# Kernel tuning notes

Hardware: AMD Instinct MI355X
Metric: run time of the kernel (lower is better)

Reference implementation:

```python
import jax, jax.numpy as jnp
import numpy as np

K = 0.15
MOMENTUM = 0.99998
B, C, H, W = 8, 19, 512, 1024


def setup_inputs() -> dict:
    key = jax.random.key(0)
    k1, k2 = jax.random.split(key)
    pred = jax.random.normal(k1, (B, C, H, W), dtype=jnp.float32)
    target = jax.random.randint(k2, (B, H, W), 0, C, dtype=jnp.int32)
    return {"pred": pred, "target": target, "step": 1000}


def reference(pred, target, step):
    b, c, h, w = pred.shape
    # num is a static Python int (step is a Python scalar), matching torch's int(...)
    num = int(K * b * h * w * max(MOMENTUM ** step, K))
    # per-pixel cross entropy, reduction='none': loss[b,h,w] = -log_softmax(pred)[b, target, h, w]
    logp = jax.nn.log_softmax(pred, axis=1)  # [B,C,H,W]
    loss = -jnp.take_along_axis(logp, target[:, None, :, :], axis=1)[:, 0]  # [B,H,W]
    loss = loss.reshape(-1)  # [B*H*W]
    # k-th largest loss value (torch does a full argsort; top_k suffices)
    topv = jax.lax.top_k(loss, num)[0]
    TK = topv[num - 1]
    mask = loss >= TK  # includes ties, like torch's boolean indexing
    return jnp.sum(jnp.where(mask, loss, 0.0)) / jnp.sum(mask).astype(loss.dtype)
```

## Files before the change

kernel.cpp:

```cpp
#include <hip/hip_runtime.h>

#define BB 8
#define CCH 19
#define HH 512
#define WW 1024
#define HW (HH * WW)
#define NPIX (BB * HW)
#define CHW (CCH * HW)
#define N4 (NPIX / 4)

struct SelState {
    unsigned num;
    unsigned b1, k1;
    unsigned b2, k2;
    unsigned tk_key;
};

__device__ __forceinline__ unsigned fkey(float x) {
    unsigned u = __float_as_uint(x);
    return (u & 0x80000000u) ? ~u : (u | 0x80000000u);
}

__global__ void k_num(const int* __restrict__ step_p, SelState* st) {
    if (threadIdx.x == 0 && blockIdx.x == 0) {
        int step = step_p[0];
        double m = pow(0.99998, (double)step);
        double Kc = 0.15;
        double f = m > Kc ? m : Kc;
        double v = Kc * (double)BB * (double)HH * (double)WW * f;
        st->num = (unsigned)v;
    }
}

__global__ __launch_bounds__(256) void k_loss(const float* __restrict__ pred,
                                              const int* __restrict__ target,
                                              float* __restrict__ loss) {
    int i4 = blockIdx.x * 256 + threadIdx.x;
    int p0 = i4 << 2;
    int b = p0 >> 19;
    int hw = p0 & (HW - 1);
    const float* base = pred + (size_t)b * CHW + hw;

    float4 v[CCH];
#pragma unroll
    for (int c = 0; c < CCH; ++c)
        v[c] = *reinterpret_cast<const float4*>(base + (size_t)c * HW);
    int4 tg = *reinterpret_cast<const int4*>(target + p0);

    float4 mx = v[0];
#pragma unroll
    for (int c = 1; c < CCH; ++c) {
        mx.x = fmaxf(mx.x, v[c].x);
        mx.y = fmaxf(mx.y, v[c].y);
        mx.z = fmaxf(mx.z, v[c].z);
        mx.w = fmaxf(mx.w, v[c].w);
    }
    float4 s = make_float4(0.f, 0.f, 0.f, 0.f);
    float4 xt = make_float4(0.f, 0.f, 0.f, 0.f);
#pragma unroll
    for (int c = 0; c < CCH; ++c) {
        s.x += __expf(v[c].x - mx.x);
        s.y += __expf(v[c].y - mx.y);
        s.z += __expf(v[c].z - mx.z);
        s.w += __expf(v[c].w - mx.w);
        xt.x = (tg.x == c) ? v[c].x : xt.x;
        xt.y = (tg.y == c) ? v[c].y : xt.y;
        xt.z = (tg.z == c) ? v[c].z : xt.z;
        xt.w = (tg.w == c) ? v[c].w : xt.w;
    }
    float4 o;
    o.x = __logf(s.x) + mx.x - xt.x;
    o.y = __logf(s.y) + mx.y - xt.y;
    o.z = __logf(s.z) + mx.z - xt.z;
    o.w = __logf(s.w) + mx.w - xt.w;
    *reinterpret_cast<float4*>(loss + p0) = o;
}

__global__ __launch_bounds__(256) void k_histA(const float* __restrict__ loss,
                                               unsigned* __restrict__ hist) {
    __shared__ unsigned h[2048];
    for (int i = threadIdx.x; i < 2048; i += 256) h[i] = 0;
    __syncthreads();
    int stride = gridDim.x * 256;
    for (int i4 = blockIdx.x * 256 + threadIdx.x; i4 < N4; i4 += stride) {
        float4 v = reinterpret_cast<const float4*>(loss)[i4];
        atomicAdd(&h[fkey(v.x) >> 21], 1u);
        atomicAdd(&h[fkey(v.y) >> 21], 1u);
        atomicAdd(&h[fkey(v.z) >> 21], 1u);
        atomicAdd(&h[fkey(v.w) >> 21], 1u);
    }
    __syncthreads();
    for (int i = threadIdx.x; i < 2048; i += 256) {
        unsigned c = h[i];
        if (c) atomicAdd(&hist[i], c);
    }
}

__global__ __launch_bounds__(256) void k_histB(const float* __restrict__ loss,
                                               const SelState* __restrict__ st,
                                               unsigned* __restrict__ hist) {
    __shared__ unsigned h[2048];
    for (int i = threadIdx.x; i < 2048; i += 256) h[i] = 0;
    __syncthreads();
    unsigned b1 = st->b1;
    int stride = gridDim.x * 256;
    for (int i4 = blockIdx.x * 256 + threadIdx.x; i4 < N4; i4 += stride) {
        float4 v = reinterpret_cast<const float4*>(loss)[i4];
        unsigned u;
        u = fkey(v.x); if ((u >> 21) == b1) atomicAdd(&h[(u >> 10) & 2047u], 1u);
        u = fkey(v.y); if ((u >> 21) == b1) atomicAdd(&h[(u >> 10) & 2047u], 1u);
        u = fkey(v.z); if ((u >> 21) == b1) atomicAdd(&h[(u >> 10) & 2047u], 1u);
        u = fkey(v.w); if ((u >> 21) == b1) atomicAdd(&h[(u >> 10) & 2047u], 1u);
    }
    __syncthreads();
    for (int i = threadIdx.x; i < 2048; i += 256) {
        unsigned c = h[i];
        if (c) atomicAdd(&hist[i], c);
    }
}

__global__ __launch_bounds__(256) void k_histC(const float* __restrict__ loss,
                                               const SelState* __restrict__ st,
                                               unsigned* __restrict__ hist) {
    __shared__ unsigned h[1024];
    for (int i = threadIdx.x; i < 1024; i += 256) h[i] = 0;
    __syncthreads();
    unsigned pref22 = (st->b1 << 11) | st->b2;
    int stride = gridDim.x * 256;
    for (int i4 = blockIdx.x * 256 + threadIdx.x; i4 < N4; i4 += stride) {
        float4 v = reinterpret_cast<const float4*>(loss)[i4];
        unsigned u;
        u = fkey(v.x); if ((u >> 10) == pref22) atomicAdd(&h[u & 1023u], 1u);
        u = fkey(v.y); if ((u >> 10) == pref22) atomicAdd(&h[u & 1023u], 1u);
        u = fkey(v.z); if ((u >> 10) == pref22) atomicAdd(&h[u & 1023u], 1u);
        u = fkey(v.w); if ((u >> 10) == pref22) atomicAdd(&h[u & 1023u], 1u);
    }
    __syncthreads();
    for (int i = threadIdx.x; i < 1024; i += 256) {
        unsigned c = h[i];
        if (c) atomicAdd(&hist[i], c);
    }
}

template <int NBINS, int PASS>
__global__ __launch_bounds__(256) void k_scan(const unsigned* __restrict__ hist,
                                              SelState* st) {
    constexpr int PER = NBINS / 256;
    __shared__ unsigned chunk[256];
    int t = threadIdx.x;
    unsigned k = (PASS == 0) ? st->num : (PASS == 1 ? st->k1 : st->k2);

    unsigned local[PER];
    unsigned lsum = 0;
#pragma unroll
    for (int j = 0; j < PER; ++j) { local[j] = hist[t * PER + j]; lsum += local[j]; }
    chunk[t] = lsum;
    __syncthreads();
    for (int off = 1; off < 256; off <<= 1) {
        unsigned add = (t + off < 256) ? chunk[t + off] : 0u;
        __syncthreads();
        chunk[t] += add;
        __syncthreads();
    }
    unsigned cum = (t < 255) ? chunk[t + 1] : 0u;
#pragma unroll
    for (int j = PER - 1; j >= 0; --j) {
        unsigned c = local[j];
        if (k > cum && k <= cum + c) {
            unsigned bin = (unsigned)(t * PER + j);
            unsigned krem = k - cum;
            if (PASS == 0) { st->b1 = bin; st->k1 = krem; }
            else if (PASS == 1) { st->b2 = bin; st->k2 = krem; }
            else { st->tk_key = (st->b1 << 21) | (st->b2 << 10) | bin; }
        }
        cum += c;
    }
}

__global__ __launch_bounds__(256) void k_final(const float* __restrict__ loss,
                                               const SelState* __restrict__ st,
                                               double* __restrict__ psum,
                                               unsigned* __restrict__ pcnt) {
    unsigned tk = st->tk_key;
    double sum = 0.0;
    unsigned cnt = 0;
    int stride = gridDim.x * 256;
    for (int i4 = blockIdx.x * 256 + threadIdx.x; i4 < N4; i4 += stride) {
        float4 v = reinterpret_cast<const float4*>(loss)[i4];
        if (fkey(v.x) >= tk) { sum += (double)v.x; cnt++; }
        if (fkey(v.y) >= tk) { sum += (double)v.y; cnt++; }
        if (fkey(v.z) >= tk) { sum += (double)v.z; cnt++; }
        if (fkey(v.w) >= tk) { sum += (double)v.w; cnt++; }
    }
#pragma unroll
    for (int off = 32; off >= 1; off >>= 1) {
        sum += __shfl_down(sum, off);
        cnt += __shfl_down(cnt, off);
    }
    __shared__ double wsum[4];
    __shared__ unsigned wcnt[4];
    int wid = threadIdx.x >> 6, lane = threadIdx.x & 63;
    if (lane == 0) { wsum[wid] = sum; wcnt[wid] = cnt; }
    __syncthreads();
    if (threadIdx.x == 0) {
        psum[blockIdx.x] = wsum[0] + wsum[1] + wsum[2] + wsum[3];
        pcnt[blockIdx.x] = wcnt[0] + wcnt[1] + wcnt[2] + wcnt[3];
    }
}

__global__ __launch_bounds__(256) void k_finalize(const double* __restrict__ psum,
                                                  const unsigned* __restrict__ pcnt,
                                                  float* __restrict__ out, int nblocks) {
    double s = 0.0;
    unsigned long long c = 0;
    for (int i = threadIdx.x; i < nblocks; i += 256) { s += psum[i]; c += pcnt[i]; }
#pragma unroll
    for (int off = 32; off >= 1; off >>= 1) {
        s += __shfl_down(s, off);
        c += __shfl_down(c, off);
    }
    __shared__ double wsum[4];
    __shared__ unsigned long long wcnt[4];
    int wid = threadIdx.x >> 6, lane = threadIdx.x & 63;
    if (lane == 0) { wsum[wid] = s; wcnt[wid] = c; }
    __syncthreads();
    if (threadIdx.x == 0) {
        double ts = wsum[0] + wsum[1] + wsum[2] + wsum[3];
        unsigned long long tc = wcnt[0] + wcnt[1] + wcnt[2] + wcnt[3];
        out[0] = (float)(ts / (double)tc);
    }
}

extern "C" void kernel_launch(void* const* d_in, const int* in_sizes, int n_in,
                              void* d_out, int out_size, void* d_ws, size_t ws_size,
                              hipStream_t stream) {
    const float* pred = (const float*)d_in[0];
    const int* target = (const int*)d_in[1];
    const int* step = (const int*)d_in[2];
    float* out = (float*)d_out;

    char* ws = (char*)d_ws;
    const size_t LOSS_BYTES = (size_t)NPIX * 4;
    float* loss = (float*)ws;
    unsigned* hist1 = (unsigned*)(ws + LOSS_BYTES);
    unsigned* hist2 = hist1 + 2048;
    unsigned* hist3 = hist2 + 2048;
    SelState* st = (SelState*)(hist3 + 1024);
    double* psum = (double*)(ws + LOSS_BYTES + 20480 + 32);
    unsigned* pcnt = (unsigned*)(psum + 1024);

    hipMemsetAsync(hist1, 0, 20480, stream);

    k_num<<<1, 1, 0, stream>>>(step, st);
    k_loss<<<N4 / 256, 256, 0, stream>>>(pred, target, loss);
    k_histA<<<1024, 256, 0, stream>>>(loss, hist1);
    k_scan<2048, 0><<<1, 256, 0, stream>>>(hist1, st);
    k_histB<<<1024, 256, 0, stream>>>(loss, st, hist2);
    k_scan<2048, 1><<<1, 256, 0, stream>>>(hist2, st);
    k_histC<<<1024, 256, 0, stream>>>(loss, st, hist3);
    k_scan<1024, 2><<<1, 256, 0, stream>>>(hist3, st);
    k_final<<<1024, 256, 0, stream>>>(loss, st, psum, pcnt);
    k_finalize<<<1, 256, 0, stream>>>(psum, pcnt, out, 1024);
}
```

Measured before the change: 138.2 us.

## Fuse loss with first histogram and fold final masked sum into third pass

Computes per-pixel cross-entropy and the first radix histogram in one grid-stride kernel, which removes a full read of the loss buffer. The third histogram pass now also accumulates fixed-point sums and counts for values above the prefix and per-bin sums within it. That lets a single-block kernel finish selection and compute the mean without another pass over the loss. The memset and the separate final and finalize kernels are replaced by a small init kernel. In exchange it adds 64-bit shared and global atomics and fixed-point summation, which assumes non-negative losses and has limited precision.

```diff
diff --git a/kernel.cpp b/kernel.cpp
--- a/kernel.cpp
+++ b/kernel.cpp
@@ -9,11 +9,12 @@
 #define CHW (CCH * HW)
 #define N4 (NPIX / 4)
 
+#define FIX_SCALE 17179869184.0
+
 struct SelState {
     unsigned num;
     unsigned b1, k1;
     unsigned b2, k2;
-    unsigned tk_key;
 };
 
 __device__ __forceinline__ unsigned fkey(float x) {
@@ -21,73 +22,76 @@
     return (u & 0x80000000u) ? ~u : (u | 0x80000000u);
 }
 
-__global__ void k_num(const int* __restrict__ step_p, SelState* st) {
-    if (threadIdx.x == 0 && blockIdx.x == 0) {
+__device__ __forceinline__ unsigned long long fix64(float x) {
+    return (unsigned long long)((double)x * FIX_SCALE);
+}
+
+__global__ __launch_bounds__(256) void k_init(const int* __restrict__ step_p,
+                                              unsigned* __restrict__ zbase,
+                                              SelState* st) {
+    for (int i = threadIdx.x; i < 7172; i += 256) zbase[i] = 0u;
+    if (threadIdx.x == 0) {
         int step = step_p[0];
         double m = pow(0.99998, (double)step);
         double Kc = 0.15;
         double f = m > Kc ? m : Kc;
-        double v = Kc * (double)BB * (double)HH * (double)WW * f;
-        st->num = (unsigned)v;
-    }
-}
-
-__global__ __launch_bounds__(256) void k_loss(const float* __restrict__ pred,
-                                              const int* __restrict__ target,
-                                              float* __restrict__ loss) {
-    int i4 = blockIdx.x * 256 + threadIdx.x;
-    int p0 = i4 << 2;
-    int b = p0 >> 19;
-    int hw = p0 & (HW - 1);
-    const float* base = pred + (size_t)b * CHW + hw;
-
-    float4 v[CCH];
-#pragma unroll
-    for (int c = 0; c < CCH; ++c)
-        v[c] = *reinterpret_cast<const float4*>(base + (size_t)c * HW);
-    int4 tg = *reinterpret_cast<const int4*>(target + p0);
-
-    float4 mx = v[0];
-#pragma unroll
-    for (int c = 1; c < CCH; ++c) {
-        mx.x = fmaxf(mx.x, v[c].x);
-        mx.y = fmaxf(mx.y, v[c].y);
-        mx.z = fmaxf(mx.z, v[c].z);
-        mx.w = fmaxf(mx.w, v[c].w);
-    }
-    float4 s = make_float4(0.f, 0.f, 0.f, 0.f);
-    float4 xt = make_float4(0.f, 0.f, 0.f, 0.f);
-#pragma unroll
-    for (int c = 0; c < CCH; ++c) {
-        s.x += __expf(v[c].x - mx.x);
-        s.y += __expf(v[c].y - mx.y);
-        s.z += __expf(v[c].z - mx.z);
-        s.w += __expf(v[c].w - mx.w);
-        xt.x = (tg.x == c) ? v[c].x : xt.x;
-        xt.y = (tg.y == c) ? v[c].y : xt.y;
-        xt.z = (tg.z == c) ? v[c].z : xt.z;
-        xt.w = (tg.w == c) ? v[c].w : xt.w;
-    }
-    float4 o;
-    o.x = __logf(s.x) + mx.x - xt.x;
-    o.y = __logf(s.y) + mx.y - xt.y;
-    o.z = __logf(s.z) + mx.z - xt.z;
-    o.w = __logf(s.w) + mx.w - xt.w;
-    *reinterpret_cast<float4*>(loss + p0) = o;
-}
-
-__global__ __launch_bounds__(256) void k_histA(const float* __restrict__ loss,
-                                               unsigned* __restrict__ hist) {
+        st->num = (unsigned)(Kc * (double)BB * (double)HH * (double)WW * f);
+    }
+}
+
+__global__ __launch_bounds__(256) void k_loss_hist(const float* __restrict__ pred,
+                                                   const int* __restrict__ target,
+                                                   float* __restrict__ loss,
+                                                   unsigned* __restrict__ hist) {
     __shared__ unsigned h[2048];
     for (int i = threadIdx.x; i < 2048; i += 256) h[i] = 0;
     __syncthreads();
+
     int stride = gridDim.x * 256;
     for (int i4 = blockIdx.x * 256 + threadIdx.x; i4 < N4; i4 += stride) {
-        float4 v = reinterpret_cast<const float4*>(loss)[i4];
-        atomicAdd(&h[fkey(v.x) >> 21], 1u);
-        atomicAdd(&h[fkey(v.y) >> 21], 1u);
-        atomicAdd(&h[fkey(v.z) >> 21], 1u);
-        atomicAdd(&h[fkey(v.w) >> 21], 1u);
+        int p0 = i4 << 2;
+        int b = p0 >> 19;
+        int hw = p0 & (HW - 1);
+        const float* base = pred + (size_t)b * CHW + hw;
+
+        float4 v[CCH];
+#pragma unroll
+        for (int c = 0; c < CCH; ++c)
+            v[c] = *reinterpret_cast<const float4*>(base + (size_t)c * HW);
+        int4 tg = *reinterpret_cast<const int4*>(target + p0);
+
+        float4 mx = v[0];
+#pragma unroll
+        for (int c = 1; c < CCH; ++c) {
+            mx.x = fmaxf(mx.x, v[c].x);
+            mx.y = fmaxf(mx.y, v[c].y);
+            mx.z = fmaxf(mx.z, v[c].z);
+            mx.w = fmaxf(mx.w, v[c].w);
+        }
+        float4 s = make_float4(0.f, 0.f, 0.f, 0.f);
+        float4 xt = make_float4(0.f, 0.f, 0.f, 0.f);
+#pragma unroll
+        for (int c = 0; c < CCH; ++c) {
+            s.x += __expf(v[c].x - mx.x);
+            s.y += __expf(v[c].y - mx.y);
+            s.z += __expf(v[c].z - mx.z);
+            s.w += __expf(v[c].w - mx.w);
+            xt.x = (tg.x == c) ? v[c].x : xt.x;
+            xt.y = (tg.y == c) ? v[c].y : xt.y;
+            xt.z = (tg.z == c) ? v[c].z : xt.z;
+            xt.w = (tg.w == c) ? v[c].w : xt.w;
+        }
+        float4 o;
+        o.x = __logf(s.x) + mx.x - xt.x;
+        o.y = __logf(s.y) + mx.y - xt.y;
+        o.z = __logf(s.z) + mx.z - xt.z;
+        o.w = __logf(s.w) + mx.w - xt.w;
+        *reinterpret_cast<float4*>(loss + p0) = o;
+
+        atomicAdd(&h[fkey(o.x) >> 21], 1u);
+        atomicAdd(&h[fkey(o.y) >> 21], 1u);
+        atomicAdd(&h[fkey(o.z) >> 21], 1u);
+        atomicAdd(&h[fkey(o.w) >> 21], 1u);
     }
     __syncthreads();
     for (int i = threadIdx.x; i < 2048; i += 256) {
@@ -121,39 +125,68 @@
 
 __global__ __launch_bounds__(256) void k_histC(const float* __restrict__ loss,
                                                const SelState* __restrict__ st,
-                                               unsigned* __restrict__ hist) {
+                                               unsigned* __restrict__ h3g,
+                                               unsigned long long* __restrict__ bsg,
+                                               unsigned long long* __restrict__ aboveSum,
+                                               unsigned* __restrict__ aboveCnt) {
     __shared__ unsigned h[1024];
-    for (int i = threadIdx.x; i < 1024; i += 256) h[i] = 0;
+    __shared__ unsigned long long bs[1024];
+    for (int i = threadIdx.x; i < 1024; i += 256) { h[i] = 0; bs[i] = 0ull; }
     __syncthreads();
     unsigned pref22 = (st->b1 << 11) | st->b2;
+    unsigned long long asum = 0ull;
+    unsigned acnt = 0;
     int stride = gridDim.x * 256;
     for (int i4 = blockIdx.x * 256 + threadIdx.x; i4 < N4; i4 += stride) {
         float4 v = reinterpret_cast<const float4*>(loss)[i4];
-        unsigned u;
-        u = fkey(v.x); if ((u >> 10) == pref22) atomicAdd(&h[u & 1023u], 1u);
-        u = fkey(v.y); if ((u >> 10) == pref22) atomicAdd(&h[u & 1023u], 1u);
-        u = fkey(v.z); if ((u >> 10) == pref22) atomicAdd(&h[u & 1023u], 1u);
-        u = fkey(v.w); if ((u >> 10) == pref22) atomicAdd(&h[u & 1023u], 1u);
+        unsigned u, p;
+        u = fkey(v.x); p = u >> 10;
+        if (p > pref22) { asum += fix64(v.x); acnt++; }
+        else if (p == pref22) { atomicAdd(&h[u & 1023u], 1u); atomicAdd(&bs[u & 1023u], fix64(v.x)); }
+        u = fkey(v.y); p = u >> 10;
+        if (p > pref22) { asum += fix64(v.y); acnt++; }
+        else if (p == pref22) { atomicAdd(&h[u & 1023u], 1u); atomicAdd(&bs[u & 1023u], fix64(v.y)); }
+        u = fkey(v.z); p = u >> 10;
+        if (p > pref22) { asum += fix64(v.z); acnt++; }
+        else if (p == pref22) { atomicAdd(&h[u & 1023u], 1u); atomicAdd(&bs[u & 1023u], fix64(v.z)); }
+        u = fkey(v.w); p = u >> 10;
+        if (p > pref22) { asum += fix64(v.w); acnt++; }
+        else if (p == pref22) { atomicAdd(&h[u & 1023u], 1u); atomicAdd(&bs[u & 1023u], fix64(v.w)); }
+    }
+#pragma unroll
+    for (int off = 32; off >= 1; off >>= 1) {
+        asum += __shfl_down(asum, off);
+        acnt += __shfl_down(acnt, off);
+    }
+    __shared__ unsigned long long wsum[4];
+    __shared__ unsigned wcnt[4];
+    int wid = threadIdx.x >> 6, lane = threadIdx.x & 63;
+    if (lane == 0) { wsum[wid] = asum; wcnt[wid] = acnt; }
+    __syncthreads();
+    if (threadIdx.x == 0) {
+        unsigned long long ts = wsum[0] + wsum[1] + wsum[2] + wsum[3];
+        unsigned tc = wcnt[0] + wcnt[1] + wcnt[2] + wcnt[3];
+        if (ts) atomicAdd(aboveSum, ts);
+        if (tc) atomicAdd(aboveCnt, tc);
     }
     __syncthreads();
     for (int i = threadIdx.x; i < 1024; i += 256) {
         unsigned c = h[i];
-        if (c) atomicAdd(&hist[i], c);
-    }
-}
-
-template <int NBINS, int PASS>
+        if (c) { atomicAdd(&h3g[i], c); atomicAdd(&bsg[i], bs[i]); }
+    }
+}
+
+template <int PASS>
 __global__ __launch_bounds__(256) void k_scan(const unsigned* __restrict__ hist,
                                               SelState* st) {
-    constexpr int PER = NBINS / 256;
     __shared__ unsigned chunk[256];
     int t = threadIdx.x;
-    unsigned k = (PASS == 0) ? st->num : (PASS == 1 ? st->k1 : st->k2);
-
-    unsigned local[PER];
+    unsigned k = (PASS == 0) ? st->num : st->k1;
+
+    unsigned local[8];
     unsigned lsum = 0;
 #pragma unroll
-    for (int j = 0; j < PER; ++j) { local[j] = hist[t * PER + j]; lsum += local[j]; }
+    for (int j = 0; j < 8; ++j) { local[j] = hist[t * 8 + j]; lsum += local[j]; }
     chunk[t] = lsum;
     __syncthreads();
     for (int off = 1; off < 256; off <<= 1) {
@@ -164,70 +197,73 @@
     }
     unsigned cum = (t < 255) ? chunk[t + 1] : 0u;
 #pragma unroll
-    for (int j = PER - 1; j >= 0; --j) {
+    for (int j = 7; j >= 0; --j) {
         unsigned c = local[j];
         if (k > cum && k <= cum + c) {
-            unsigned bin = (unsigned)(t * PER + j);
+            unsigned bin = (unsigned)(t * 8 + j);
             unsigned krem = k - cum;
             if (PASS == 0) { st->b1 = bin; st->k1 = krem; }
-            else if (PASS == 1) { st->b2 = bin; st->k2 = krem; }
-            else { st->tk_key = (st->b1 << 21) | (st->b2 << 10) | bin; }
+            else { st->b2 = bin; st->k2 = krem; }
         }
         cum += c;
     }
 }
 
-__global__ __launch_bounds__(256) void k_final(const float* __restrict__ loss,
-                                               const SelState* __restrict__ st,
-                                               double* __restrict__ psum,
-                                               unsigned* __restrict__ pcnt) {
-    unsigned tk = st->tk_key;
-    double sum = 0.0;
+__global__ __launch_bounds__(256) void k_last(const unsigned* __restrict__ h3,
+                                              const unsigned long long* __restrict__ bsg,
+                                              const unsigned long long* __restrict__ aboveSum,
+                                              const unsigned* __restrict__ aboveCnt,
+                                              const SelState* __restrict__ st,
+                                              float* __restrict__ out) {
+    __shared__ unsigned chunk[256];
+    __shared__ unsigned b3sh;
+    __shared__ unsigned long long wsum[4];
+    __shared__ unsigned wcnt[4];
+    int t = threadIdx.x;
+    unsigned k = st->k2;
+
+    unsigned local[4];
+    unsigned lsum = 0;
+#pragma unroll
+    for (int j = 0; j < 4; ++j) { local[j] = h3[t * 4 + j]; lsum += local[j]; }
+    chunk[t] = lsum;
+    __syncthreads();
+    for (int off = 1; off < 256; off <<= 1) {
+        unsigned add = (t + off < 256) ? chunk[t + off] : 0u;
+        __syncthreads();
+        chunk[t] += add;
+        __syncthreads();
+    }
+    unsigned cum = (t < 255) ? chunk[t + 1] : 0u;
+#pragma unroll
+    for (int j = 3; j >= 0; --j) {
+        unsigned c = local[j];
+        if (k > cum && k <= cum + c) b3sh = (unsigned)(t * 4 + j);
+        cum += c;
+    }
+    __syncthreads();
+    unsigned b3 = b3sh;
+
+    unsigned long long s = 0ull;
     unsigned cnt = 0;
-    int stride = gridDim.x * 256;
-    for (int i4 = blockIdx.x * 256 + threadIdx.x; i4 < N4; i4 += stride) {
-        float4 v = reinterpret_cast<const float4*>(loss)[i4];
-        if (fkey(v.x) >= tk) { sum += (double)v.x; cnt++; }
-        if (fkey(v.y) >= tk) { sum += (double)v.y; cnt++; }
-        if (fkey(v.z) >= tk) { sum += (double)v.z; cnt++; }
-        if (fkey(v.w) >= tk) { sum += (double)v.w; cnt++; }
-    }
-#pragma unroll
-    for (int off = 32; off >= 1; off >>= 1) {
-        sum += __shfl_down(sum, off);
-        cnt += __shfl_down(cnt, off);
-    }
-    __shared__ double wsum[4];
-    __shared__ unsigned wcnt[4];
-    int wid = threadIdx.x >> 6, lane = threadIdx.x & 63;
-    if (lane == 0) { wsum[wid] = sum; wcnt[wid] = cnt; }
-    __syncthreads();
-    if (threadIdx.x == 0) {
-        psum[blockIdx.x] = wsum[0] + wsum[1] + wsum[2] + wsum[3];
-        pcnt[blockIdx.x] = wcnt[0] + wcnt[1] + wcnt[2] + wcnt[3];
-    }
-}
-
-__global__ __launch_bounds__(256) void k_finalize(const double* __restrict__ psum,
-                                                  const unsigned* __restrict__ pcnt,
-                                                  float* __restrict__ out, int nblocks) {
-    double s = 0.0;
-    unsigned long long c = 0;
-    for (int i = threadIdx.x; i < nblocks; i += 256) { s += psum[i]; c += pcnt[i]; }
+#pragma unroll
+    for (int j = 0; j < 4; ++j) {
+        unsigned bin = (unsigned)(t * 4 + j);
+        if (bin >= b3) { s += bsg[bin]; cnt += local[j]; }
+    }
 #pragma unroll
     for (int off = 32; off >= 1; off >>= 1) {
         s += __shfl_down(s, off);
-        c += __shfl_down(c, off);
-    }
-    __shared__ double wsum[4];
-    __shared__ unsigned long long wcnt[4];
-    int wid = threadIdx.x >> 6, lane = threadIdx.x & 63;
-    if (lane == 0) { wsum[wid] = s; wcnt[wid] = c; }
-    __syncthreads();
-    if (threadIdx.x == 0) {
-        double ts = wsum[0] + wsum[1] + wsum[2] + wsum[3];
-        unsigned long long tc = wcnt[0] + wcnt[1] + wcnt[2] + wcnt[3];
-        out[0] = (float)(ts / (double)tc);
+        cnt += __shfl_down(cnt, off);
+    }
+    int wid = t >> 6, lane = t & 63;
+    if (lane == 0) { wsum[wid] = s; wcnt[wid] = cnt; }
+    __syncthreads();
+    if (t == 0) {
+        unsigned long long ts = wsum[0] + wsum[1] + wsum[2] + wsum[3] + aboveSum[0];
+        unsigned long long tc = (unsigned long long)(wcnt[0] + wcnt[1] + wcnt[2] + wcnt[3])
+                              + (unsigned long long)aboveCnt[0];
+        out[0] = (float)(((double)ts / FIX_SCALE) / (double)tc);
     }
 }
 
@@ -242,23 +278,20 @@
     char* ws = (char*)d_ws;
     const size_t LOSS_BYTES = (size_t)NPIX * 4;
     float* loss = (float*)ws;
-    unsigned* hist1 = (unsigned*)(ws + LOSS_BYTES);
-    unsigned* hist2 = hist1 + 2048;
-    unsigned* hist3 = hist2 + 2048;
-    SelState* st = (SelState*)(hist3 + 1024);
-    double* psum = (double*)(ws + LOSS_BYTES + 20480 + 32);
-    unsigned* pcnt = (unsigned*)(psum + 1024);
-
-    hipMemsetAsync(hist1, 0, 20480, stream);
-
-    k_num<<<1, 1, 0, stream>>>(step, st);
-    k_loss<<<N4 / 256, 256, 0, stream>>>(pred, target, loss);
-    k_histA<<<1024, 256, 0, stream>>>(loss, hist1);
-    k_scan<2048, 0><<<1, 256, 0, stream>>>(hist1, st);
+    char* sb = ws + LOSS_BYTES;
+    unsigned* hist1 = (unsigned*)(sb);
+    unsigned* hist2 = (unsigned*)(sb + 8192);
+    unsigned* h3 = (unsigned*)(sb + 16384);
+    unsigned long long* bs = (unsigned long long*)(sb + 20480);
+    unsigned long long* aboveSum = (unsigned long long*)(sb + 28672);
+    unsigned* aboveCnt = (unsigned*)(sb + 28680);
+    SelState* st = (SelState*)(sb + 28688);
+
+    k_init<<<1, 256, 0, stream>>>(step, hist1, st);
+    k_loss_hist<<<1024, 256, 0, stream>>>(pred, target, loss, hist1);
+    k_scan<0><<<1, 256, 0, stream>>>(hist1, st);
     k_histB<<<1024, 256, 0, stream>>>(loss, st, hist2);
-    k_scan<2048, 1><<<1, 256, 0, stream>>>(hist2, st);
-    k_histC<<<1024, 256, 0, stream>>>(loss, st, hist3);
-    k_scan<1024, 2><<<1, 256, 0, stream>>>(hist3, st);
-    k_final<<<1024, 256, 0, stream>>>(loss, st, psum, pcnt);
-    k_finalize<<<1, 256, 0, stream>>>(psum, pcnt, out, 1024);
-}
+    k_scan<1><<<1, 256, 0, stream>>>(hist2, st);
+    k_histC<<<1024, 256, 0, stream>>>(loss, st, h3, bs, aboveSum, aboveCnt);
+    k_last<<<1, 256, 0, stream>>>(h3, bs, aboveSum, aboveCnt, st, out);
+}
```

Result: slower. 141.4 us (+2.3%).
